# Performance work log

Hardware: AMD Instinct MI355X
Metric: run time of the kernel (lower is better)

The kernel has to match this reference:

```python
import jax, jax.numpy as jnp
import numpy as np

N, E, F_IN, H, D = 50000, 800000, 128, 4, 32


def setup_inputs() -> dict:
    key = jax.random.key(0)
    k_x, k_e, k_w, k_al, k_ar = jax.random.split(key, 5)
    x = jax.random.normal(k_x, (N, F_IN), dtype=jnp.float32)
    edge_index = jax.random.randint(k_e, (2, E), 0, N, dtype=jnp.int32).astype(jnp.int64)
    # xavier-uniform-like scales
    s_w = float(np.sqrt(6.0 / (F_IN + H * D)))
    s_a = float(np.sqrt(6.0 / (D + 1)))
    W = jax.random.uniform(k_w, (F_IN, H * D), jnp.float32, -s_w, s_w)
    att_l = jax.random.uniform(k_al, (H, D), jnp.float32, -s_a, s_a)
    att_r = jax.random.uniform(k_ar, (H, D), jnp.float32, -s_a, s_a)
    bias = jnp.zeros((H * D,), jnp.float32)
    return {"x": x, "edge_index": edge_index, "W": W, "att_l": att_l, "att_r": att_r, "bias": bias}


def reference(x, edge_index, W, att_l, att_r, bias):
    num_nodes = x.shape[0]
    n_heads, head_dim = att_l.shape
    h = (x @ W).reshape(num_nodes, n_heads, head_dim)          # [N,H,D]
    alpha_l = jnp.einsum('nhd,hd->nh', h, att_l)               # [N,H]
    alpha_r = jnp.einsum('nhd,hd->nh', h, att_r)               # [N,H]
    from_idx, to_idx = edge_index[0], edge_index[1]
    att = alpha_l[from_idx] + alpha_r[to_idx]                  # [E,H]
    att = jax.nn.leaky_relu(att, negative_slope=0.2)
    # segment softmax over edges grouped by destination node (shift by global
    # per-head max, exactly as the source's _softmax effectively does)
    att = att - jax.lax.stop_gradient(jnp.max(att, axis=0, keepdims=True))
    ex = jnp.exp(att)                                          # [E,H]
    denom = jax.ops.segment_sum(ex, to_idx, num_segments=num_nodes)  # [N,H]
    att_n = ex / (denom[to_idx] + 1e-9)                        # [E,H]
    # scatter-weighted aggregation: out[n] = sum_{e: to=n} att[e] * h[from[e]]
    msgs = att_n[:, :, None] * h[from_idx]                     # [E,H,D]
    out = jax.ops.segment_sum(msgs, to_idx, num_segments=num_nodes)  # [N,H,D]
    out = out.reshape(num_nodes, n_heads * head_dim) + bias
    return out
```

## Files before the change

### kernel.cpp

```cpp
#include <hip/hip_runtime.h>
#include <cstdint>

#define N_NODES 50000
#define N_EDGES 800000
#define F_IN    128
#define N_HEADS 4
#define HEAD_DIM 32
#define F_OUT   128

#define NBUCK   391
#define NPB     128
#define KA_GRID 512
#define EPB     1563
#define EPB_PAD 1568
#define REC_CAP 2560
#define STAGE_CAP REC_CAP
#define NSTRIP  (N_NODES / 16)
#define NGEMM   ((NSTRIP + 3) / 4)

typedef unsigned int uint32;
typedef unsigned short ushort;
typedef __attribute__((ext_vector_type(8))) short short8v;
typedef __attribute__((ext_vector_type(4))) float float4v;

typedef __attribute__((address_space(1))) const ushort gushort;
typedef __attribute__((address_space(3))) ushort lushort;

__device__ __forceinline__ ushort f2bf(float f) {
    uint32 u = __float_as_uint(f);
    return (ushort)((u + 0x7FFFu + ((u >> 16) & 1u)) >> 16);
}


__device__ __forceinline__ int block_scan_excl_256(int v, int* p_total)
{
    const int t = threadIdx.x, lane = t & 63, wv = t >> 6;
    int incl = v;
#pragma unroll
    for (int d = 1; d < 64; d <<= 1) {
        int u = __shfl_up(incl, d);
        if (lane >= d) incl += u;
    }
    __shared__ int wsum[4];
    if (lane == 63) wsum[wv] = incl;
    __syncthreads();
    int woff = 0;
#pragma unroll
    for (int j = 0; j < 4; ++j) {
        int s = wsum[j];
        if (j < wv) woff += s;
    }
    if (p_total) *p_total = wsum[0] + wsum[1] + wsum[2] + wsum[3];
    __syncthreads();
    return woff + incl - v;
}

__global__ __launch_bounds__(256) void k_prep(const float* __restrict__ W,
    ushort* __restrict__ WTF)
{
    const int id = blockIdx.x * 256 + threadIdx.x;
    if (id >= 32 * 64) return;
    const int tile = id >> 6, l = id & 63;
    const int q = l >> 4, c15 = l & 15;
    const int nt = tile >> 2, kt = tile & 3;
    short8v hv, lv;
#pragma unroll
    for (int j = 0; j < 8; ++j) {
        const int k = kt * 32 + q * 8 + j;
        const float w = W[k * F_OUT + nt * 16 + c15];
        const ushort hi = f2bf(w);
        const float hif = __uint_as_float((uint32)hi << 16);
        hv[j] = (short)hi;
        lv[j] = (short)f2bf(w - hif);
    }
    *(short8v*)&WTF[tile * 512 + l * 8]         = hv;
    *(short8v*)&WTF[16384 + tile * 512 + l * 8] = lv;
}

__global__ __launch_bounds__(256, 2) void k_bin_gemm(
    const int* __restrict__ ei, const float* __restrict__ x,
    const ushort* __restrict__ WTF,
    const float* __restrict__ attl, const float* __restrict__ attr,
    uint32* __restrict__ blockarr, int* __restrict__ cnts, int* __restrict__ offs,
    uint32* __restrict__ hbq, float* __restrict__ aLp, float* __restrict__ aRp)
{
    __shared__ __attribute__((aligned(16))) char lds_buf[65536];

    if (blockIdx.x < KA_GRID) {
        int*    cur = (int*)lds_buf;
        int*    off = cur + 512;
        uint32* stg = (uint32*)(off + 512);
        const int sb = blockIdx.x, t = threadIdx.x;

        cur[t] = 0; cur[t + 256] = 0;
        __syncthreads();

        const int e0 = sb * EPB;
        const int lim = min(EPB, N_EDGES - e0);
        for (int i = t; i < lim; i += 256)
            atomicAdd(&cur[ei[N_EDGES + e0 + i] >> 7], 1);
        __syncthreads();

        const int c0 = cur[2 * t], c1 = cur[2 * t + 1];
        const int ex = block_scan_excl_256(c0 + c1, nullptr);
        off[2 * t]     = ex;
        off[2 * t + 1] = ex + c0;
        __syncthreads();

        for (int bb = t; bb < NBUCK; bb += 256) {
            cnts[(size_t)bb * KA_GRID + sb] = cur[bb];
            offs[(size_t)bb * KA_GRID + sb] = off[bb];
        }
        __syncthreads();

        for (int i = t; i < lim; i += 256) {
            const int from = ei[e0 + i];
            const int to   = ei[N_EDGES + e0 + i];
            const int pos = atomicAdd(&off[to >> 7], 1);
            stg[pos] = (uint32)from | ((uint32)(to & 127) << 16);
        }
        __syncthreads();

        uint32* dst = blockarr + (size_t)sb * EPB_PAD;
        for (int i = t; i < lim; i += 256)
            dst[i] = stg[i];
        return;
    }

    const int bid   = blockIdx.x - KA_GRID;
    const int lane  = threadIdx.x & 63;
    const int wv    = threadIdx.x >> 6;
    const int q     = lane >> 4;
    const int c15   = lane & 15;

    ushort* wt = (ushort*)lds_buf;
#pragma unroll
    for (int i = 0; i < 16; ++i) {
        const int chunk = wv * 16 + i;
        __builtin_amdgcn_global_load_lds(
            (gushort*)(WTF + chunk * 512 + lane * 8),
            (lushort*)(wt + chunk * 512), 16, 0, 0);
    }
    __syncthreads();

    const int strip = bid * 4 + wv;
    if (strip >= NSTRIP) return;
    const int row0 = strip * 16;

    const float* xrow = x + (size_t)(row0 + c15) * F_IN + q * 8;
    short8v ahi[4], alo[4];
#pragma unroll
    for (int kt = 0; kt < 4; ++kt) {
        const float4 f0 = *(const float4*)(xrow + kt * 32);
        const float4 f1 = *(const float4*)(xrow + kt * 32 + 4);
        const float fs[8] = {f0.x, f0.y, f0.z, f0.w, f1.x, f1.y, f1.z, f1.w};
#pragma unroll
        for (int j = 0; j < 8; ++j) {
            const ushort hi = f2bf(fs[j]);
            const float hif = __uint_as_float((uint32)hi << 16);
            ahi[kt][j] = (short)hi;
            alo[kt][j] = (short)f2bf(fs[j] - hif);
        }
    }

    float4v acc[8];
#pragma unroll
    for (int nt = 0; nt < 8; ++nt) {
        float4v a = {0.f, 0.f, 0.f, 0.f};
#pragma unroll
        for (int kt = 0; kt < 4; ++kt) {
            const short8v bh = *(const short8v*)(wt + (nt * 4 + kt) * 512 + lane * 8);
            const short8v bl = *(const short8v*)(wt + 16384 + (nt * 4 + kt) * 512 + lane * 8);
            a = __builtin_amdgcn_mfma_f32_16x16x32_bf16(ahi[kt], bh, a, 0, 0, 0);
            a = __builtin_amdgcn_mfma_f32_16x16x32_bf16(alo[kt], bh, a, 0, 0, 0);
            a = __builtin_amdgcn_mfma_f32_16x16x32_bf16(ahi[kt], bl, a, 0, 0, 0);
        }
        acc[nt] = a;
    }

#pragma unroll
    for (int nt = 0; nt < 4; ++nt) {
#pragma unroll
        for (int r = 0; r < 4; ++r) {
            const uint32 d = (uint32)f2bf(acc[nt][r]) | ((uint32)f2bf(acc[nt + 4][r]) << 16);
            hbq[(size_t)(row0 + q * 4 + r) * 64 + nt * 16 + c15] = d;
        }
    }

    float aLacc[4][4] = {{0.f}}, aRacc[4][4] = {{0.f}};
#pragma unroll
    for (int nt = 0; nt < 8; ++nt) {
        const float alv = attl[nt * 16 + c15];
        const float arv = attr[nt * 16 + c15];
        const int hh = nt >> 1;
#pragma unroll
        for (int r = 0; r < 4; ++r) {
            aLacc[r][hh] = fmaf(acc[nt][r], alv, aLacc[r][hh]);
            aRacc[r][hh] = fmaf(acc[nt][r], arv, aRacc[r][hh]);
        }
    }
#pragma unroll
    for (int r = 0; r < 4; ++r) {
#pragma unroll
        for (int hh = 0; hh < 4; ++hh) {
            float vl = aLacc[r][hh], vr = aRacc[r][hh];
#pragma unroll
            for (int d = 1; d < 16; d <<= 1) {
                vl += __shfl_xor(vl, d);
                vr += __shfl_xor(vr, d);
            }
            if (c15 == hh) {
                const int row = row0 + q * 4 + r;
                const int pos = (hh & 1) * 2 + (hh >> 1);
                aLp[row * N_HEADS + pos] = vl;
                aRp[row * N_HEADS + pos] = vr;
            }
        }
    }
}

__global__ __launch_bounds__(256) void k_build(const uint32* __restrict__ blockarr,
    const int* __restrict__ cnts, const int* __restrict__ offs,
    int* __restrict__ count, int* __restrict__ offsets, int* __restrict__ rec_from)
{
    __shared__ uint32 stage[STAGE_CAP];
    __shared__ int hist[NPB], curn[NPB];
    const int b = blockIdx.x, t = threadIdx.x;

    int c[2], o[2];
#pragma unroll
    for (int j = 0; j < 2; ++j) {
        c[j] = cnts[(size_t)b * KA_GRID + 2 * t + j];
        o[j] = offs[(size_t)b * KA_GRID + 2 * t + j];
    }
    int total;
    int ex = block_scan_excl_256(c[0] + c[1], &total);
    if (t < NPB) hist[t] = 0;
    __syncthreads();

#pragma unroll
    for (int j = 0; j < 2; ++j) {
        const int sb = 2 * t + j;
        const uint32* src = blockarr + (size_t)sb * EPB_PAD + o[j];
        for (int i = 0; i < c[j]; ++i) {
            const int p = ex + i;
            if (p < STAGE_CAP) stage[p] = src[i];
        }
        ex += c[j];
    }
    __syncthreads();

    const int S = min(total, STAGE_CAP);
    for (int i = t; i < S; i += 256) atomicAdd(&hist[stage[i] >> 16], 1);
    __syncthreads();

    const int hv = (t < NPB) ? hist[t] : 0;
    int tot2;
    const int lo = block_scan_excl_256(hv, &tot2);
    const int rbase = b * REC_CAP;
    const int n = b * NPB + t;
    if (t < NPB && n < N_NODES) {
        count[n]   = hv;
        offsets[n] = rbase + lo;
    }
    if (t < NPB) curn[t] = lo;
    __syncthreads();

    for (int i = t; i < S; i += 256) {
        const uint32 e = stage[i];
        const int pos = atomicAdd(&curn[e >> 16], 1);
        rec_from[rbase + pos] = (int)(e & 0xFFFFu);
    }
}

__global__ __launch_bounds__(256) void k_agg(const int* __restrict__ rec_from,
    const int* __restrict__ count, const int* __restrict__ offsets,
    const float* __restrict__ aLp, const float* __restrict__ aRp,
    const uint32* __restrict__ hbq,
    const float* __restrict__ bias, float* __restrict__ out)
{
    const int lane = threadIdx.x & 63;
    const int n = blockIdx.x * 4 + (threadIdx.x >> 6);
    if (n >= N_NODES) return;
    const int cnt  = count[n];
    const int off  = offsets[n];
    const int hsel = (lane >> 5) * 2;
    const int l31  = lane & 31;
    const int gsel = lane & 32;
    const float2 arv = *(const float2*)&aRp[n * N_HEADS + hsel];
    float ax = 0.f, ay = 0.f, ds0 = 0.f, ds1 = 0.f;

    for (int base = 0; base < cnt; base += 32) {
        const int m = min(32, cnt - base);
        int vf = 0;
        float e0p = 0.f, e1p = 0.f;
        if (l31 < m) {
            vf = rec_from[off + base + l31];
            const float2 af = *(const float2*)&aLp[vf * N_HEADS + hsel];
            float t0 = af.x + arv.x; t0 = (t0 > 0.f) ? t0 : 0.2f * t0;
            float t1 = af.y + arv.y; t1 = (t1 > 0.f) ? t1 : 0.2f * t1;
            e0p = __expf(t0);
            e1p = __expf(t1);
        }
        int i = 0;
        for (; i + 8 <= m; i += 8) {
            int f[8]; uint32 h[8]; float e0[8], e1[8];
#pragma unroll
            for (int j = 0; j < 8; ++j) {
                const int s = gsel | (i + j);
                f[j]  = __shfl(vf, s);
                e0[j] = __shfl(e0p, s);
                e1[j] = __shfl(e1p, s);
            }
#pragma unroll
            for (int j = 0; j < 8; ++j) h[j] = hbq[(size_t)f[j] * 64 + lane];
#pragma unroll
            for (int j = 0; j < 8; ++j) {
                ax = fmaf(e0[j], __uint_as_float(h[j] << 16), ax);
                ay = fmaf(e1[j], __uint_as_float(h[j] & 0xFFFF0000u), ay);
                ds0 += e0[j]; ds1 += e1[j];
            }
        }
        for (; i + 4 <= m; i += 4) {
            int f[4]; uint32 h[4]; float e0[4], e1[4];
#pragma unroll
            for (int j = 0; j < 4; ++j) {
                const int s = gsel | (i + j);
                f[j]  = __shfl(vf, s);
                e0[j] = __shfl(e0p, s);
                e1[j] = __shfl(e1p, s);
            }
#pragma unroll
            for (int j = 0; j < 4; ++j) h[j] = hbq[(size_t)f[j] * 64 + lane];
#pragma unroll
            for (int j = 0; j < 4; ++j) {
                ax = fmaf(e0[j], __uint_as_float(h[j] << 16), ax);
                ay = fmaf(e1[j], __uint_as_float(h[j] & 0xFFFF0000u), ay);
                ds0 += e0[j]; ds1 += e1[j];
            }
        }
        for (; i < m; ++i) {
            const int s = gsel | i;
            const int f = __shfl(vf, s);
            const uint32 hv = hbq[(size_t)f * 64 + lane];
            const float e0 = __shfl(e0p, s), e1 = __shfl(e1p, s);
            ax = fmaf(e0, __uint_as_float(hv << 16), ax);
            ay = fmaf(e1, __uint_as_float(hv & 0xFFFF0000u), ay);
            ds0 += e0; ds1 += e1;
        }
    }
    const float inv0 = 1.0f / (ds0 + 1e-9f);
    const float inv1 = 1.0f / (ds1 + 1e-9f);
    out[n * F_OUT + lane]      = ax * inv0 + bias[lane];
    out[n * F_OUT + 64 + lane] = ay * inv1 + bias[64 + lane];
}

extern "C" void kernel_launch(void* const* d_in, const int* in_sizes, int n_in,
                              void* d_out, int out_size, void* d_ws, size_t ws_size,
                              hipStream_t stream)
{
    const float* x    = (const float*)d_in[0];
    const int*   ei   = (const int*)d_in[1];
    const float* W    = (const float*)d_in[2];
    const float* attl = (const float*)d_in[3];
    const float* attr = (const float*)d_in[4];
    const float* bias = (const float*)d_in[5];
    float* out = (float*)d_out;

    char* p = (char*)d_ws;
    auto carve = [&](size_t bytes) -> char* {
        char* q = p;
        p += (bytes + 255) & ~size_t(255);
        return q;
    };
    uint32* hbq      = (uint32*)carve((size_t)N_NODES * 64 * 4);
    uint32* blockarr = (uint32*)carve((size_t)KA_GRID * EPB_PAD * 4);
    int*    rec_from = (int*)carve((size_t)NBUCK * REC_CAP * 4);
    ushort* WTF      = (ushort*)carve(32768 * 2);
    float*  aLp      = (float*)carve((size_t)N_NODES * N_HEADS * 4);
    float*  aRp      = (float*)carve((size_t)N_NODES * N_HEADS * 4);
    int*    cnts     = (int*)carve((size_t)NBUCK * KA_GRID * 4);
    int*    offs     = (int*)carve((size_t)NBUCK * KA_GRID * 4);
    int*    count    = (int*)carve((size_t)N_NODES * 4);
    int*    offsets  = (int*)carve((size_t)N_NODES * 4);

    k_prep<<<8, 256, 0, stream>>>(W, WTF);
    k_bin_gemm<<<KA_GRID + NGEMM, 256, 0, stream>>>(ei, x, WTF,
                                                    attl, attr, blockarr,
                                                    cnts, offs,
                                                    hbq, aLp, aRp);
    k_build<<<NBUCK, 256, 0, stream>>>(blockarr, cnts, offs,
                                       count, offsets, rec_from);
    k_agg<<<(N_NODES + 3) / 4, 256, 0, stream>>>(rec_from, count, offsets,
                                                 aLp, aRp, hbq, bias, out);
}
```

Before: 154.3 us.

## Precompute edge attention exponentials and softmax denominators in CSR build kernel

Moves the leaky-relu plus exp attention computation and the per-destination denominator sum from the aggregation kernel into the bucket build kernel. There, destination alpha values and the denominators live in shared memory, and per-edge exp weights are written to a new workspace array alongside rec_from. The aggregation kernel then reads indices and weights directly instead of using shuffles, drops its running denominator sums, and scalarizes count and offset with readfirstlane. In exchange it writes and reads an extra 16 bytes of weights per edge and adds shared-memory float atomics in the build kernel.

```diff
diff --git a/kernel.cpp b/kernel.cpp
--- a/kernel.cpp
+++ b/kernel.cpp
@@ -221,11 +221,23 @@
 
 __global__ __launch_bounds__(256) void k_build(const uint32* __restrict__ blockarr,
     const int* __restrict__ cnts, const int* __restrict__ offs,
-    int* __restrict__ count, int* __restrict__ offsets, int* __restrict__ rec_from)
+    const float* __restrict__ aLp, const float* __restrict__ aRp,
+    int* __restrict__ count, int* __restrict__ offsets, int* __restrict__ rec_from,
+    float* __restrict__ wexp, float* __restrict__ dinv)
 {
     __shared__ uint32 stage[STAGE_CAP];
     __shared__ int hist[NPB], curn[NPB];
+    __shared__ float aR[NPB * 4];
+    __shared__ float denom[NPB * 4];
     const int b = blockIdx.x, t = threadIdx.x;
+
+    if (t < NPB) {
+        const int n = b * NPB + t;
+        float4 v = make_float4(0.f, 0.f, 0.f, 0.f);
+        if (n < N_NODES) v = *(const float4*)&aRp[(size_t)n * 4];
+        *(float4*)&aR[t * 4] = v;
+    }
+    denom[t] = 0.f; denom[t + 256] = 0.f;
 
     int c[2], o[2];
 #pragma unroll
@@ -268,91 +280,90 @@
 
     for (int i = t; i < S; i += 256) {
         const uint32 e = stage[i];
-        const int pos = atomicAdd(&curn[e >> 16], 1);
-        rec_from[rbase + pos] = (int)(e & 0xFFFFu);
+        const int toloc = e >> 16;
+        const int from  = (int)(e & 0xFFFFu);
+        const int pos = atomicAdd(&curn[toloc], 1);
+        const float4 al = *(const float4*)&aLp[(size_t)from * 4];
+        const float4 ar = *(const float4*)&aR[toloc * 4];
+        float t0 = al.x + ar.x; t0 = (t0 > 0.f) ? t0 : 0.2f * t0;
+        float t1 = al.y + ar.y; t1 = (t1 > 0.f) ? t1 : 0.2f * t1;
+        float t2 = al.z + ar.z; t2 = (t2 > 0.f) ? t2 : 0.2f * t2;
+        float t3 = al.w + ar.w; t3 = (t3 > 0.f) ? t3 : 0.2f * t3;
+        const float e0 = __expf(t0), e1 = __expf(t1);
+        const float e2 = __expf(t2), e3 = __expf(t3);
+        rec_from[rbase + pos] = from;
+        *(float4*)&wexp[(size_t)(rbase + pos) * 4] = make_float4(e0, e1, e2, e3);
+        atomicAdd(&denom[toloc * 4 + 0], e0);
+        atomicAdd(&denom[toloc * 4 + 1], e1);
+        atomicAdd(&denom[toloc * 4 + 2], e2);
+        atomicAdd(&denom[toloc * 4 + 3], e3);
+    }
+    __syncthreads();
+
+    if (t < NPB && n < N_NODES) {
+        const float4 d = *(const float4*)&denom[t * 4];
+        *(float4*)&dinv[(size_t)n * 4] = make_float4(
+            1.0f / (d.x + 1e-9f), 1.0f / (d.y + 1e-9f),
+            1.0f / (d.z + 1e-9f), 1.0f / (d.w + 1e-9f));
     }
 }
 
 __global__ __launch_bounds__(256) void k_agg(const int* __restrict__ rec_from,
     const int* __restrict__ count, const int* __restrict__ offsets,
-    const float* __restrict__ aLp, const float* __restrict__ aRp,
+    const float* __restrict__ dinv, const float* __restrict__ wexp,
     const uint32* __restrict__ hbq,
     const float* __restrict__ bias, float* __restrict__ out)
 {
     const int lane = threadIdx.x & 63;
     const int n = blockIdx.x * 4 + (threadIdx.x >> 6);
     if (n >= N_NODES) return;
-    const int cnt  = count[n];
-    const int off  = offsets[n];
+    const int cnt = __builtin_amdgcn_readfirstlane(count[n]);
+    const int off = __builtin_amdgcn_readfirstlane(offsets[n]);
     const int hsel = (lane >> 5) * 2;
-    const int l31  = lane & 31;
-    const int gsel = lane & 32;
-    const float2 arv = *(const float2*)&aRp[n * N_HEADS + hsel];
-    float ax = 0.f, ay = 0.f, ds0 = 0.f, ds1 = 0.f;
-
-    for (int base = 0; base < cnt; base += 32) {
-        const int m = min(32, cnt - base);
-        int vf = 0;
-        float e0p = 0.f, e1p = 0.f;
-        if (l31 < m) {
-            vf = rec_from[off + base + l31];
-            const float2 af = *(const float2*)&aLp[vf * N_HEADS + hsel];
-            float t0 = af.x + arv.x; t0 = (t0 > 0.f) ? t0 : 0.2f * t0;
-            float t1 = af.y + arv.y; t1 = (t1 > 0.f) ? t1 : 0.2f * t1;
-            e0p = __expf(t0);
-            e1p = __expf(t1);
-        }
-        int i = 0;
-        for (; i + 8 <= m; i += 8) {
-            int f[8]; uint32 h[8]; float e0[8], e1[8];
-#pragma unroll
-            for (int j = 0; j < 8; ++j) {
-                const int s = gsel | (i + j);
-                f[j]  = __shfl(vf, s);
-                e0[j] = __shfl(e0p, s);
-                e1[j] = __shfl(e1p, s);
-            }
-#pragma unroll
-            for (int j = 0; j < 8; ++j) h[j] = hbq[(size_t)f[j] * 64 + lane];
-#pragma unroll
-            for (int j = 0; j < 8; ++j) {
-                ax = fmaf(e0[j], __uint_as_float(h[j] << 16), ax);
-                ay = fmaf(e1[j], __uint_as_float(h[j] & 0xFFFF0000u), ay);
-                ds0 += e0[j]; ds1 += e1[j];
-            }
-        }
-        for (; i + 4 <= m; i += 4) {
-            int f[4]; uint32 h[4]; float e0[4], e1[4];
-#pragma unroll
-            for (int j = 0; j < 4; ++j) {
-                const int s = gsel | (i + j);
-                f[j]  = __shfl(vf, s);
-                e0[j] = __shfl(e0p, s);
-                e1[j] = __shfl(e1p, s);
-            }
-#pragma unroll
-            for (int j = 0; j < 4; ++j) h[j] = hbq[(size_t)f[j] * 64 + lane];
-#pragma unroll
-            for (int j = 0; j < 4; ++j) {
-                ax = fmaf(e0[j], __uint_as_float(h[j] << 16), ax);
-                ay = fmaf(e1[j], __uint_as_float(h[j] & 0xFFFF0000u), ay);
-                ds0 += e0[j]; ds1 += e1[j];
-            }
-        }
-        for (; i < m; ++i) {
-            const int s = gsel | i;
-            const int f = __shfl(vf, s);
-            const uint32 hv = hbq[(size_t)f * 64 + lane];
-            const float e0 = __shfl(e0p, s), e1 = __shfl(e1p, s);
-            ax = fmaf(e0, __uint_as_float(hv << 16), ax);
-            ay = fmaf(e1, __uint_as_float(hv & 0xFFFF0000u), ay);
-            ds0 += e0; ds1 += e1;
-        }
-    }
-    const float inv0 = 1.0f / (ds0 + 1e-9f);
-    const float inv1 = 1.0f / (ds1 + 1e-9f);
-    out[n * F_OUT + lane]      = ax * inv0 + bias[lane];
-    out[n * F_OUT + 64 + lane] = ay * inv1 + bias[64 + lane];
+    const int epair = hsel >> 1;
+    const float2* wex2 = (const float2*)wexp;
+
+    float ax = 0.f, ay = 0.f;
+    int i = 0;
+    for (; i + 8 <= cnt; i += 8) {
+        int f[8]; uint32 h[8]; float2 e[8];
+#pragma unroll
+        for (int j = 0; j < 8; ++j) f[j] = rec_from[off + i + j];
+#pragma unroll
+        for (int j = 0; j < 8; ++j) h[j] = hbq[(size_t)f[j] * 64 + lane];
+#pragma unroll
+        for (int j = 0; j < 8; ++j) e[j] = wex2[(size_t)(off + i + j) * 2 + epair];
+#pragma unroll
+        for (int j = 0; j < 8; ++j) {
+            ax = fmaf(e[j].x, __uint_as_float(h[j] << 16), ax);
+            ay = fmaf(e[j].y, __uint_as_float(h[j] & 0xFFFF0000u), ay);
+        }
+    }
+    for (; i + 4 <= cnt; i += 4) {
+        int f[4]; uint32 h[4]; float2 e[4];
+#pragma unroll
+        for (int j = 0; j < 4; ++j) f[j] = rec_from[off + i + j];
+#pragma unroll
+        for (int j = 0; j < 4; ++j) h[j] = hbq[(size_t)f[j] * 64 + lane];
+#pragma unroll
+        for (int j = 0; j < 4; ++j) e[j] = wex2[(size_t)(off + i + j) * 2 + epair];
+#pragma unroll
+        for (int j = 0; j < 4; ++j) {
+            ax = fmaf(e[j].x, __uint_as_float(h[j] << 16), ax);
+            ay = fmaf(e[j].y, __uint_as_float(h[j] & 0xFFFF0000u), ay);
+        }
+    }
+    for (; i < cnt; ++i) {
+        const int f = rec_from[off + i];
+        const uint32 hv = hbq[(size_t)f * 64 + lane];
+        const float2 e = wex2[(size_t)(off + i) * 2 + epair];
+        ax = fmaf(e.x, __uint_as_float(hv << 16), ax);
+        ay = fmaf(e.y, __uint_as_float(hv & 0xFFFF0000u), ay);
+    }
+
+    const float2 iv = *(const float2*)&dinv[(size_t)n * 4 + hsel];
+    out[n * F_OUT + lane]      = ax * iv.x + bias[lane];
+    out[n * F_OUT + 64 + lane] = ay * iv.y + bias[64 + lane];
 }
 
 extern "C" void kernel_launch(void* const* d_in, const int* in_sizes, int n_in,
@@ -376,9 +387,11 @@
     uint32* hbq      = (uint32*)carve((size_t)N_NODES * 64 * 4);
     uint32* blockarr = (uint32*)carve((size_t)KA_GRID * EPB_PAD * 4);
     int*    rec_from = (int*)carve((size_t)NBUCK * REC_CAP * 4);
+    float*  wexp     = (float*)carve((size_t)NBUCK * REC_CAP * 4 * 4);
     ushort* WTF      = (ushort*)carve(32768 * 2);
     float*  aLp      = (float*)carve((size_t)N_NODES * N_HEADS * 4);
     float*  aRp      = (float*)carve((size_t)N_NODES * N_HEADS * 4);
+    float*  dinv     = (float*)carve((size_t)N_NODES * N_HEADS * 4);
     int*    cnts     = (int*)carve((size_t)NBUCK * KA_GRID * 4);
     int*    offs     = (int*)carve((size_t)NBUCK * KA_GRID * 4);
     int*    count    = (int*)carve((size_t)N_NODES * 4);
@@ -389,8 +402,8 @@
                                                     attl, attr, blockarr,
                                                     cnts, offs,
                                                     hbq, aLp, aRp);
-    k_build<<<NBUCK, 256, 0, stream>>>(blockarr, cnts, offs,
-                                       count, offsets, rec_from);
+    k_build<<<NBUCK, 256, 0, stream>>>(blockarr, cnts, offs, aLp, aRp,
+                                       count, offsets, rec_from, wexp, dinv);
     k_agg<<<(N_NODES + 3) / 4, 256, 0, stream>>>(rec_from, count, offsets,
-                                                 aLp, aRp, hbq, bias, out);
-}
+                                                 dinv, wexp, hbq, bias, out);
+}
```

Result: slower. 177.2 us (+14.9%).

## Regroup stages: fuse weight prep into binning, co-schedule GEMM with CSR build

Applied to the files above, without the earlier changes.

Replaces the four-launch chain (prep, bin+GEMM, build, agg) with three launches. The weight bf16 split now runs as extra blocks of the edge-binning kernel. The CSR bucket build runs interleaved with the GEMM blocks in one grid, with every third block doing a build. This removes one launch and its dependency gap, and lets the LDS-heavy build overlap with the MFMA GEMM instead of running alone. In exchange the GEMM no longer overlaps with edge binning, which now runs as its own kernel.

```diff
diff --git a/kernel.cpp b/kernel.cpp
--- a/kernel.cpp
+++ b/kernel.cpp
@@ -17,6 +17,7 @@
 #define STAGE_CAP REC_CAP
 #define NSTRIP  (N_NODES / 16)
 #define NGEMM   ((NSTRIP + 3) / 4)
+#define GB_GRID (NGEMM + NBUCK)
 
 typedef unsigned int uint32;
 typedef unsigned short ushort;
@@ -55,79 +56,136 @@
     return woff + incl - v;
 }
 
-__global__ __launch_bounds__(256) void k_prep(const float* __restrict__ W,
-    ushort* __restrict__ WTF)
-{
-    const int id = blockIdx.x * 256 + threadIdx.x;
-    if (id >= 32 * 64) return;
-    const int tile = id >> 6, l = id & 63;
-    const int q = l >> 4, c15 = l & 15;
-    const int nt = tile >> 2, kt = tile & 3;
-    short8v hv, lv;
-#pragma unroll
-    for (int j = 0; j < 8; ++j) {
-        const int k = kt * 32 + q * 8 + j;
-        const float w = W[k * F_OUT + nt * 16 + c15];
-        const ushort hi = f2bf(w);
-        const float hif = __uint_as_float((uint32)hi << 16);
-        hv[j] = (short)hi;
-        lv[j] = (short)f2bf(w - hif);
-    }
-    *(short8v*)&WTF[tile * 512 + l * 8]         = hv;
-    *(short8v*)&WTF[16384 + tile * 512 + l * 8] = lv;
-}
-
-__global__ __launch_bounds__(256, 2) void k_bin_gemm(
-    const int* __restrict__ ei, const float* __restrict__ x,
-    const ushort* __restrict__ WTF,
+__global__ __launch_bounds__(256) void k_bin_prep(
+    const int* __restrict__ ei, const float* __restrict__ W,
+    ushort* __restrict__ WTF,
+    uint32* __restrict__ blockarr, int* __restrict__ cnts, int* __restrict__ offs)
+{
+    __shared__ int cur[512];
+    __shared__ int off[512];
+    __shared__ uint32 stg[EPB];
+
+    if (blockIdx.x >= KA_GRID) {
+        const int id = (blockIdx.x - KA_GRID) * 256 + threadIdx.x;
+        if (id >= 32 * 64) return;
+        const int tile = id >> 6, l = id & 63;
+        const int q = l >> 4, c15 = l & 15;
+        const int nt = tile >> 2, kt = tile & 3;
+        short8v hv, lv;
+#pragma unroll
+        for (int j = 0; j < 8; ++j) {
+            const int k = kt * 32 + q * 8 + j;
+            const float w = W[k * F_OUT + nt * 16 + c15];
+            const ushort hi = f2bf(w);
+            const float hif = __uint_as_float((uint32)hi << 16);
+            hv[j] = (short)hi;
+            lv[j] = (short)f2bf(w - hif);
+        }
+        *(short8v*)&WTF[tile * 512 + l * 8]         = hv;
+        *(short8v*)&WTF[16384 + tile * 512 + l * 8] = lv;
+        return;
+    }
+
+    const int sb = blockIdx.x, t = threadIdx.x;
+
+    cur[t] = 0; cur[t + 256] = 0;
+    __syncthreads();
+
+    const int e0 = sb * EPB;
+    const int lim = min(EPB, N_EDGES - e0);
+    for (int i = t; i < lim; i += 256)
+        atomicAdd(&cur[ei[N_EDGES + e0 + i] >> 7], 1);
+    __syncthreads();
+
+    const int c0 = cur[2 * t], c1 = cur[2 * t + 1];
+    const int ex = block_scan_excl_256(c0 + c1, nullptr);
+    off[2 * t]     = ex;
+    off[2 * t + 1] = ex + c0;
+    __syncthreads();
+
+    for (int bb = t; bb < NBUCK; bb += 256) {
+        cnts[(size_t)bb * KA_GRID + sb] = cur[bb];
+        offs[(size_t)bb * KA_GRID + sb] = off[bb];
+    }
+    __syncthreads();
+
+    for (int i = t; i < lim; i += 256) {
+        const int from = ei[e0 + i];
+        const int to   = ei[N_EDGES + e0 + i];
+        const int pos = atomicAdd(&off[to >> 7], 1);
+        stg[pos] = (uint32)from | ((uint32)(to & 127) << 16);
+    }
+    __syncthreads();
+
+    uint32* dst = blockarr + (size_t)sb * EPB_PAD;
+    for (int i = t; i < lim; i += 256)
+        dst[i] = stg[i];
+}
+
+__global__ __launch_bounds__(256, 2) void k_gemm_build(
+    const float* __restrict__ x, const ushort* __restrict__ WTF,
     const float* __restrict__ attl, const float* __restrict__ attr,
-    uint32* __restrict__ blockarr, int* __restrict__ cnts, int* __restrict__ offs,
-    uint32* __restrict__ hbq, float* __restrict__ aLp, float* __restrict__ aRp)
+    const uint32* __restrict__ blockarr,
+    const int* __restrict__ cnts, const int* __restrict__ offs,
+    uint32* __restrict__ hbq, float* __restrict__ aLp, float* __restrict__ aRp,
+    int* __restrict__ count, int* __restrict__ offsets, int* __restrict__ rec_from)
 {
     __shared__ __attribute__((aligned(16))) char lds_buf[65536];
 
-    if (blockIdx.x < KA_GRID) {
-        int*    cur = (int*)lds_buf;
-        int*    off = cur + 512;
-        uint32* stg = (uint32*)(off + 512);
-        const int sb = blockIdx.x, t = threadIdx.x;
-
-        cur[t] = 0; cur[t + 256] = 0;
+    if (blockIdx.x % 3 == 0) {
+        uint32* stage = (uint32*)lds_buf;
+        int*    hist  = (int*)(lds_buf + STAGE_CAP * 4);
+        int*    curn  = hist + NPB;
+        const int b = blockIdx.x / 3, t = threadIdx.x;
+
+        int c[2], o[2];
+#pragma unroll
+        for (int j = 0; j < 2; ++j) {
+            c[j] = cnts[(size_t)b * KA_GRID + 2 * t + j];
+            o[j] = offs[(size_t)b * KA_GRID + 2 * t + j];
+        }
+        int total;
+        int ex = block_scan_excl_256(c[0] + c[1], &total);
+        if (t < NPB) hist[t] = 0;
         __syncthreads();
 
-        const int e0 = sb * EPB;
-        const int lim = min(EPB, N_EDGES - e0);
-        for (int i = t; i < lim; i += 256)
-            atomicAdd(&cur[ei[N_EDGES + e0 + i] >> 7], 1);
+#pragma unroll
+        for (int j = 0; j < 2; ++j) {
+            const int sb = 2 * t + j;
+            const uint32* src = blockarr + (size_t)sb * EPB_PAD + o[j];
+            for (int i = 0; i < c[j]; ++i) {
+                const int p = ex + i;
+                if (p < STAGE_CAP) stage[p] = src[i];
+            }
+            ex += c[j];
+        }
         __syncthreads();
 
-        const int c0 = cur[2 * t], c1 = cur[2 * t + 1];
-        const int ex = block_scan_excl_256(c0 + c1, nullptr);
-        off[2 * t]     = ex;
-        off[2 * t + 1] = ex + c0;
+        const int S = min(total, STAGE_CAP);
+        for (int i = t; i < S; i += 256) atomicAdd(&hist[stage[i] >> 16], 1);
         __syncthreads();
 
-        for (int bb = t; bb < NBUCK; bb += 256) {
-            cnts[(size_t)bb * KA_GRID + sb] = cur[bb];
-            offs[(size_t)bb * KA_GRID + sb] = off[bb];
-        }
+        const int hv = (t < NPB) ? hist[t] : 0;
+        int tot2;
+        const int lo = block_scan_excl_256(hv, &tot2);
+        const int rbase = b * REC_CAP;
+        const int n = b * NPB + t;
+        if (t < NPB && n < N_NODES) {
+            count[n]   = hv;
+            offsets[n] = rbase + lo;
+        }
+        if (t < NPB) curn[t] = lo;
         __syncthreads();
 
-        for (int i = t; i < lim; i += 256) {
-            const int from = ei[e0 + i];
-            const int to   = ei[N_EDGES + e0 + i];
-            const int pos = atomicAdd(&off[to >> 7], 1);
-            stg[pos] = (uint32)from | ((uint32)(to & 127) << 16);
-        }
-        __syncthreads();
-
-        uint32* dst = blockarr + (size_t)sb * EPB_PAD;
-        for (int i = t; i < lim; i += 256)
-            dst[i] = stg[i];
+        for (int i = t; i < S; i += 256) {
+            const uint32 e = stage[i];
+            const int pos = atomicAdd(&curn[e >> 16], 1);
+            rec_from[rbase + pos] = (int)(e & 0xFFFFu);
+        }
         return;
     }
 
-    const int bid   = blockIdx.x - KA_GRID;
+    const int bid   = blockIdx.x - blockIdx.x / 3 - 1;
     const int lane  = threadIdx.x & 63;
     const int wv    = threadIdx.x >> 6;
     const int q     = lane >> 4;
@@ -216,60 +274,6 @@
                 aRp[row * N_HEADS + pos] = vr;
             }
         }
-    }
-}
-
-__global__ __launch_bounds__(256) void k_build(const uint32* __restrict__ blockarr,
-    const int* __restrict__ cnts, const int* __restrict__ offs,
-    int* __restrict__ count, int* __restrict__ offsets, int* __restrict__ rec_from)
-{
-    __shared__ uint32 stage[STAGE_CAP];
-    __shared__ int hist[NPB], curn[NPB];
-    const int b = blockIdx.x, t = threadIdx.x;
-
-    int c[2], o[2];
-#pragma unroll
-    for (int j = 0; j < 2; ++j) {
-        c[j] = cnts[(size_t)b * KA_GRID + 2 * t + j];
-        o[j] = offs[(size_t)b * KA_GRID + 2 * t + j];
-    }
-    int total;
-    int ex = block_scan_excl_256(c[0] + c[1], &total);
-    if (t < NPB) hist[t] = 0;
-    __syncthreads();
-
-#pragma unroll
-    for (int j = 0; j < 2; ++j) {
-        const int sb = 2 * t + j;
-        const uint32* src = blockarr + (size_t)sb * EPB_PAD + o[j];
-        for (int i = 0; i < c[j]; ++i) {
-            const int p = ex + i;
-            if (p < STAGE_CAP) stage[p] = src[i];
-        }
-        ex += c[j];
-    }
-    __syncthreads();
-
-    const int S = min(total, STAGE_CAP);
-    for (int i = t; i < S; i += 256) atomicAdd(&hist[stage[i] >> 16], 1);
-    __syncthreads();
-
-    const int hv = (t < NPB) ? hist[t] : 0;
-    int tot2;
-    const int lo = block_scan_excl_256(hv, &tot2);
-    const int rbase = b * REC_CAP;
-    const int n = b * NPB + t;
-    if (t < NPB && n < N_NODES) {
-        count[n]   = hv;
-        offsets[n] = rbase + lo;
-    }
-    if (t < NPB) curn[t] = lo;
-    __syncthreads();
-
-    for (int i = t; i < S; i += 256) {
-        const uint32 e = stage[i];
-        const int pos = atomicAdd(&curn[e >> 16], 1);
-        rec_from[rbase + pos] = (int)(e & 0xFFFFu);
     }
 }
 
@@ -384,13 +388,11 @@
     int*    count    = (int*)carve((size_t)N_NODES * 4);
     int*    offsets  = (int*)carve((size_t)N_NODES * 4);
 
-    k_prep<<<8, 256, 0, stream>>>(W, WTF);
-    k_bin_gemm<<<KA_GRID + NGEMM, 256, 0, stream>>>(ei, x, WTF,
-                                                    attl, attr, blockarr,
-                                                    cnts, offs,
-                                                    hbq, aLp, aRp);
-    k_build<<<NBUCK, 256, 0, stream>>>(blockarr, cnts, offs,
-                                       count, offsets, rec_from);
+    k_bin_prep<<<KA_GRID + 8, 256, 0, stream>>>(ei, W, WTF, blockarr, cnts, offs);
+    k_gemm_build<<<GB_GRID, 256, 0, stream>>>(x, WTF, attl, attr,
+                                              blockarr, cnts, offs,
+                                              hbq, aLp, aRp,
+                                              count, offsets, rec_from);
     k_agg<<<(N_NODES + 3) / 4, 256, 0, stream>>>(rec_from, count, offsets,
                                                  aLp, aRp, hbq, bias, out);
 }
```

Result: faster. 149.6 us (-3.0%).
